# Kernel optimization log

Hardware: AMD Instinct MI355X
Metric: run time of the kernel (lower is better)

The kernel has to match this reference:

```python
import jax, jax.numpy as jnp
import numpy as np


def setup_inputs() -> dict:
    key = jax.random.key(0)
    k1, k2, k3, k4 = jax.random.split(key, 4)
    bs, ts0, tsk, f, nf = 1024, 32, 32, 64, 64
    return {
        "x_0": jax.random.normal(k1, (bs, ts0, f), dtype=jnp.float32),
        "x_k": jax.random.normal(k2, (bs, tsk, f), dtype=jnp.float32),
        # Conv1d weight as used: (num_filters, in_ch=1, ts_0, ts_k)
        "weight": jax.random.normal(k3, (nf, 1, ts0, tsk), dtype=jnp.float32) * 0.05,
        "bias": jax.random.normal(k4, (nf,), dtype=jnp.float32) * 0.05,
    }


def reference(x_0, x_k, weight, bias):
    bs, ts0, f = x_0.shape
    _, tsk, _ = x_k.shape
    # Outer-product interaction: (bs, f, ts_0, ts_k). This is the large HBM
    # intermediate (268 MB at these shapes) that a fused kernel would avoid.
    z = jnp.einsum('btf,byf->bfty', x_0, x_k)
    # Faithful row-major view to (bs, 1, ts_0, f*ts_k) as in torch .view.
    z = z.reshape(bs, 1, ts0, f * tsk)
    # Conv with kernel (ts_0, ts_k), stride ts_k along width; kernel height
    # equals input height so output is (bs, nf, 1, f). (Height stride is
    # irrelevant since exactly one vertical position exists.)
    out = jax.lax.conv_general_dilated(
        z, weight,
        window_strides=(tsk, tsk),
        padding='VALID',
        dimension_numbers=('NCHW', 'OIHW', 'NCHW'),
    )
    out = out + bias[None, :, None, None]
    return jnp.squeeze(out)  # (bs, num_filters, f)
```

## Files before the change

kernel.cpp:

```cpp
#include <hip/hip_runtime.h>


constexpr int ST0 = 36;
constexpr int GR  = 136;
constexpr int GB  = 32 * GR;

__global__ __launch_bounds__(1024)
__attribute__((amdgpu_waves_per_eu(4, 4)))
void cin_fused(const float* __restrict__ x0,
               const float* __restrict__ xk,
               const float* __restrict__ W,
               const float* __restrict__ bias,
               float* __restrict__ out)
{
    __shared__ __align__(16) float x0T[4 * 64 * ST0];
    __shared__ __align__(16) float Gs[4 * GB];

    const int tid  = threadIdx.x;
    const int b0   = blockIdx.x * 4;
    const int lane = tid & 63;
    const int wv   = tid >> 6;
    const int r0   = 2 * wv;

    const float4* x0src = reinterpret_cast<const float4*>(x0 + (size_t)b0 * 2048);
    const float4 a0 = x0src[tid];
    const float4 a1 = x0src[tid + 1024];

    float w0reg[32], w1reg[32];
    {
        const float4* wp = reinterpret_cast<const float4*>(W + ((size_t)lane * 32 + r0) * 32);
        #pragma unroll
        for (int q = 0; q < 8; ++q) {
            const float4 v = wp[q];
            w0reg[4*q+0] = v.x; w0reg[4*q+1] = v.y; w0reg[4*q+2] = v.z; w0reg[4*q+3] = v.w;
        }
        #pragma unroll
        for (int q = 0; q < 8; ++q) {
            const float4 v = wp[8 + q];
            w1reg[4*q+0] = v.x; w1reg[4*q+1] = v.y; w1reg[4*q+2] = v.z; w1reg[4*q+3] = v.w;
        }
    }

    {
        const int kb  = tid >> 9;
        const int u   = tid & 511;
        const int st  = u >> 4;
        const int sf4 = u & 15;
        const int sts = st ^ (4 * (sf4 & 7));
        float* rA = &x0T[(kb    ) * 64 * ST0 + (4 * sf4) * ST0];
        float* rB = &x0T[(kb + 2) * 64 * ST0 + (4 * sf4) * ST0];
        rA[0 * ST0 + sts] = a0.x; rA[1 * ST0 + sts] = a0.y;
        rA[2 * ST0 + sts] = a0.z; rA[3 * ST0 + sts] = a0.w;
        rB[0 * ST0 + sts] = a1.x; rB[1 * ST0 + sts] = a1.y;
        rB[2 * ST0 + sts] = a1.z; rB[3 * ST0 + sts] = a1.w;
    }
    __syncthreads();

    const int su = __builtin_amdgcn_readfirstlane(wv);
    for (int kb = 0; kb < 4; ++kb) {
        const float4* pk4 = reinterpret_cast<const float4*>(xk + (size_t)(b0 + kb) * 2048);
        float a00 = 0.f, a01 = 0.f, a10 = 0.f, a11 = 0.f;
        #pragma unroll
        for (int q = 0; q < 4; ++q) {
            float4 kv[8];
            #pragma unroll
            for (int m = 0; m < 8; ++m)
                kv[m] = pk4[(q * 8 + m) * 16 + su];
            #pragma unroll
            for (int m = 0; m < 8; ++m) {
                const int j = q * 8 + m;
                a00 = fmaf(w0reg[j], kv[m].x, a00);
                a01 = fmaf(w0reg[j], kv[m].y, a01);
                a10 = fmaf(w1reg[j], kv[m].z, a10);
                a11 = fmaf(w1reg[j], kv[m].w, a11);
            }
        }
        float* gb = &Gs[kb * GB];
        gb[(r0    ) * GR +      lane] = a00;
        gb[(r0    ) * GR + 68 + lane] = a01;
        gb[(r0 + 1) * GR +      lane] = a10;
        gb[(r0 + 1) * GR + 68 + lane] = a11;
    }
    __syncthreads();

    if (wv % 5 == 0) {
        const int ckb = wv / 5;
        const int l   = lane;
        const int n0  = (l >> 3) * 8;
        const int w0c = (l & 7) * 8;
        const int h   = w0c >> 5;
        const int t0  = w0c & 31;

        const float4 bva = *reinterpret_cast<const float4*>(bias + n0);
        const float4 bvb = *reinterpret_cast<const float4*>(bias + n0 + 4);

        float acc[8][8];
        #pragma unroll
        for (int i = 0; i < 8; ++i) {
            acc[0][i] = bva.x; acc[1][i] = bva.y; acc[2][i] = bva.z; acc[3][i] = bva.w;
            acc[4][i] = bvb.x; acc[5][i] = bvb.y; acc[6][i] = bvb.z; acc[7][i] = bvb.w;
        }

        const float* xbase = &x0T[ckb * 64 * ST0];
        const float* gbase = &Gs[ckb * GB + h * 68];

        #pragma unroll 4
        for (int r = 0; r < 32; ++r) {
            const int fi = 2 * r + h;
            const int p  = 4 * ((fi >> 2) & 7);
            const float4 xa = *reinterpret_cast<const float4*>(&xbase[fi * ST0 + (t0 ^ p)]);
            const float4 xb = *reinterpret_cast<const float4*>(&xbase[fi * ST0 + ((t0 + 4) ^ p)]);
            const float4 g0 = *reinterpret_cast<const float4*>(&gbase[r * GR + n0]);
            const float4 g1 = *reinterpret_cast<const float4*>(&gbase[r * GR + n0 + 4]);
            const float ge[8] = {g0.x, g0.y, g0.z, g0.w, g1.x, g1.y, g1.z, g1.w};
            const float xv[8] = {xa.x, xa.y, xa.z, xa.w, xb.x, xb.y, xb.z, xb.w};
            #pragma unroll
            for (int e = 0; e < 8; ++e)
                #pragma unroll
                for (int i = 0; i < 8; ++i)
                    acc[e][i] = fmaf(ge[e], xv[i], acc[e][i]);
        }

        float* ob = out + (size_t)(b0 + ckb) * 4096;
        #pragma unroll
        for (int e = 0; e < 8; ++e) {
            *reinterpret_cast<float4*>(&ob[(n0 + e) * 64 + w0c]) =
                make_float4(acc[e][0], acc[e][1], acc[e][2], acc[e][3]);
            *reinterpret_cast<float4*>(&ob[(n0 + e) * 64 + w0c + 4]) =
                make_float4(acc[e][4], acc[e][5], acc[e][6], acc[e][7]);
        }
    }
}

extern "C" void kernel_launch(void* const* d_in, const int* in_sizes, int n_in,
                              void* d_out, int out_size, void* d_ws, size_t ws_size,
                              hipStream_t stream) {
    const float* x0   = (const float*)d_in[0];
    const float* xk   = (const float*)d_in[1];
    const float* W    = (const float*)d_in[2];
    const float* bias = (const float*)d_in[3];
    float* out = (float*)d_out;

    cin_fused<<<dim3(256), dim3(1024), 0, stream>>>(x0, xk, W, bias, out);
}
```

Measured before the change: 95.67 us.

## Use packed fp16 dot2 for second stage, reorder weights, spread across all waves

Stores x0 and the intermediate G in shared memory as packed fp16 pairs and computes the second contraction with fdot2, so all 16 waves participate instead of only 4 (wv%5==0). A separate pre-kernel reorders the weight tensor into the workspace so weight register loads are coalesced. The barrier after the x0 shared store is removed, relying on the later barrier. This lowers precision of the intermediate and inputs to fp16 (round-toward-zero), risking accuracy, and adds an extra kernel launch.

```diff
diff --git a/kernel.cpp b/kernel.cpp
--- a/kernel.cpp
+++ b/kernel.cpp
@@ -1,26 +1,35 @@
 #include <hip/hip_runtime.h>
 
 
-constexpr int ST0 = 36;
-constexpr int GR  = 136;
-constexpr int GB  = 32 * GR;
+typedef __fp16 hh2 __attribute__((ext_vector_type(2)));
+
+constexpr int XPS = 36;
+
+__global__ __launch_bounds__(256)
+void w_reorder(const float4* __restrict__ W4, float4* __restrict__ Wt)
+{
+    const int o    = blockIdx.x * 256 + threadIdx.x;
+    const int lane = o & 63;
+    const int q    = (o >> 6) & 15;
+    const int wv   = o >> 10;
+    Wt[o] = W4[lane * 256 + (2 * wv + (q >> 3)) * 8 + (q & 7)];
+}
 
 __global__ __launch_bounds__(1024)
 __attribute__((amdgpu_waves_per_eu(4, 4)))
 void cin_fused(const float* __restrict__ x0,
                const float* __restrict__ xk,
-               const float* __restrict__ W,
+               const float4* __restrict__ Wt,
                const float* __restrict__ bias,
                float* __restrict__ out)
 {
-    __shared__ __align__(16) float x0T[4 * 64 * ST0];
-    __shared__ __align__(16) float Gs[4 * GB];
+    __shared__ __align__(16) hh2 xP[4][2][16][XPS];
+    __shared__ __align__(16) hh2 Gp[4][2][16][64];
 
     const int tid  = threadIdx.x;
     const int b0   = blockIdx.x * 4;
     const int lane = tid & 63;
     const int wv   = tid >> 6;
-    const int r0   = 2 * wv;
 
     const float4* x0src = reinterpret_cast<const float4*>(x0 + (size_t)b0 * 2048);
     const float4 a0 = x0src[tid];
@@ -28,44 +37,40 @@
 
     float w0reg[32], w1reg[32];
     {
-        const float4* wp = reinterpret_cast<const float4*>(W + ((size_t)lane * 32 + r0) * 32);
+        const float4* wp = Wt + (size_t)wv * 1024 + lane;
         #pragma unroll
         for (int q = 0; q < 8; ++q) {
-            const float4 v = wp[q];
+            const float4 v = wp[q * 64];
             w0reg[4*q+0] = v.x; w0reg[4*q+1] = v.y; w0reg[4*q+2] = v.z; w0reg[4*q+3] = v.w;
         }
         #pragma unroll
         for (int q = 0; q < 8; ++q) {
-            const float4 v = wp[8 + q];
+            const float4 v = wp[(q + 8) * 64];
             w1reg[4*q+0] = v.x; w1reg[4*q+1] = v.y; w1reg[4*q+2] = v.z; w1reg[4*q+3] = v.w;
         }
     }
 
     {
-        const int kb  = tid >> 9;
-        const int u   = tid & 511;
-        const int st  = u >> 4;
-        const int sf4 = u & 15;
-        const int sts = st ^ (4 * (sf4 & 7));
-        float* rA = &x0T[(kb    ) * 64 * ST0 + (4 * sf4) * ST0];
-        float* rB = &x0T[(kb + 2) * 64 * ST0 + (4 * sf4) * ST0];
-        rA[0 * ST0 + sts] = a0.x; rA[1 * ST0 + sts] = a0.y;
-        rA[2 * ST0 + sts] = a0.z; rA[3 * ST0 + sts] = a0.w;
-        rB[0 * ST0 + sts] = a1.x; rB[1 * ST0 + sts] = a1.y;
-        rB[2 * ST0 + sts] = a1.z; rB[3 * ST0 + sts] = a1.w;
+        const int kb = tid >> 9;
+        const int u  = tid & 511;
+        const int t  = u >> 4;
+        const int f  = u & 15;
+        xP[kb    ][0][f][t] = __builtin_amdgcn_cvt_pkrtz(a0.x, a0.z);
+        xP[kb    ][1][f][t] = __builtin_amdgcn_cvt_pkrtz(a0.y, a0.w);
+        xP[kb + 2][0][f][t] = __builtin_amdgcn_cvt_pkrtz(a1.x, a1.z);
+        xP[kb + 2][1][f][t] = __builtin_amdgcn_cvt_pkrtz(a1.y, a1.w);
     }
-    __syncthreads();
 
     const int su = __builtin_amdgcn_readfirstlane(wv);
     for (int kb = 0; kb < 4; ++kb) {
-        const float4* pk4 = reinterpret_cast<const float4*>(xk + (size_t)(b0 + kb) * 2048);
+        const float4* pk4 = reinterpret_cast<const float4*>(xk + (size_t)(b0 + kb) * 2048) + su;
         float a00 = 0.f, a01 = 0.f, a10 = 0.f, a11 = 0.f;
         #pragma unroll
         for (int q = 0; q < 4; ++q) {
             float4 kv[8];
             #pragma unroll
             for (int m = 0; m < 8; ++m)
-                kv[m] = pk4[(q * 8 + m) * 16 + su];
+                kv[m] = pk4[(q * 8 + m) * 16];
             #pragma unroll
             for (int m = 0; m < 8; ++m) {
                 const int j = q * 8 + m;
@@ -75,59 +80,50 @@
                 a11 = fmaf(w1reg[j], kv[m].w, a11);
             }
         }
-        float* gb = &Gs[kb * GB];
-        gb[(r0    ) * GR +      lane] = a00;
-        gb[(r0    ) * GR + 68 + lane] = a01;
-        gb[(r0 + 1) * GR +      lane] = a10;
-        gb[(r0 + 1) * GR + 68 + lane] = a11;
+        Gp[kb][0][wv][lane] = __builtin_amdgcn_cvt_pkrtz(a00, a10);
+        Gp[kb][1][wv][lane] = __builtin_amdgcn_cvt_pkrtz(a01, a11);
     }
     __syncthreads();
 
-    if (wv % 5 == 0) {
-        const int ckb = wv / 5;
-        const int l   = lane;
-        const int n0  = (l >> 3) * 8;
-        const int w0c = (l & 7) * 8;
+    {
+        const int kb  = tid >> 8;
+        const int t2  = tid & 255;
+        const int n0  = (t2 >> 4) * 4;
+        const int w0c = (t2 & 15) * 4;
         const int h   = w0c >> 5;
         const int t0  = w0c & 31;
 
-        const float4 bva = *reinterpret_cast<const float4*>(bias + n0);
-        const float4 bvb = *reinterpret_cast<const float4*>(bias + n0 + 4);
-
-        float acc[8][8];
+        const float4 bv = *reinterpret_cast<const float4*>(bias + n0);
+        float acc[4][4];
         #pragma unroll
-        for (int i = 0; i < 8; ++i) {
-            acc[0][i] = bva.x; acc[1][i] = bva.y; acc[2][i] = bva.z; acc[3][i] = bva.w;
-            acc[4][i] = bvb.x; acc[5][i] = bvb.y; acc[6][i] = bvb.z; acc[7][i] = bvb.w;
+        for (int i = 0; i < 4; ++i) {
+            acc[0][i] = bv.x; acc[1][i] = bv.y; acc[2][i] = bv.z; acc[3][i] = bv.w;
         }
 
-        const float* xbase = &x0T[ckb * 64 * ST0];
-        const float* gbase = &Gs[ckb * GB + h * 68];
-
-        #pragma unroll 4
-        for (int r = 0; r < 32; ++r) {
-            const int fi = 2 * r + h;
-            const int p  = 4 * ((fi >> 2) & 7);
-            const float4 xa = *reinterpret_cast<const float4*>(&xbase[fi * ST0 + (t0 ^ p)]);
-            const float4 xb = *reinterpret_cast<const float4*>(&xbase[fi * ST0 + ((t0 + 4) ^ p)]);
-            const float4 g0 = *reinterpret_cast<const float4*>(&gbase[r * GR + n0]);
-            const float4 g1 = *reinterpret_cast<const float4*>(&gbase[r * GR + n0 + 4]);
-            const float ge[8] = {g0.x, g0.y, g0.z, g0.w, g1.x, g1.y, g1.z, g1.w};
-            const float xv[8] = {xa.x, xa.y, xa.z, xa.w, xb.x, xb.y, xb.z, xb.w};
+        #pragma unroll
+        for (int rp = 0; rp < 16; ++rp) {
+            union { float4 f; hh2 p[4]; } xu, guv;
+            xu.f  = *reinterpret_cast<const float4*>(&xP[kb][h][rp][t0]);
+            guv.f = *reinterpret_cast<const float4*>(&Gp[kb][h][rp][n0]);
             #pragma unroll
-            for (int e = 0; e < 8; ++e)
+            for (int e = 0; e < 4; ++e) {
                 #pragma unroll
-                for (int i = 0; i < 8; ++i)
-                    acc[e][i] = fmaf(ge[e], xv[i], acc[e][i]);
+                for (int i = 0; i < 4; ++i) {
+#if __has_builtin(__builtin_amdgcn_fdot2)
+                    acc[e][i] = __builtin_amdgcn_fdot2(guv.p[e], xu.p[i], acc[e][i], false);
+#else
+                    acc[e][i] += (float)guv.p[e].x * (float)xu.p[i].x
+                               + (float)guv.p[e].y * (float)xu.p[i].y;
+#endif
+                }
+            }
         }
 
-        float* ob = out + (size_t)(b0 + ckb) * 4096;
+        float* ob = out + (size_t)(b0 + kb) * 4096;
         #pragma unroll
-        for (int e = 0; e < 8; ++e) {
+        for (int e = 0; e < 4; ++e) {
             *reinterpret_cast<float4*>(&ob[(n0 + e) * 64 + w0c]) =
                 make_float4(acc[e][0], acc[e][1], acc[e][2], acc[e][3]);
-            *reinterpret_cast<float4*>(&ob[(n0 + e) * 64 + w0c + 4]) =
-                make_float4(acc[e][4], acc[e][5], acc[e][6], acc[e][7]);
         }
     }
 }
@@ -140,6 +136,8 @@
     const float* W    = (const float*)d_in[2];
     const float* bias = (const float*)d_in[3];
     float* out = (float*)d_out;
+    float4* Wt = (float4*)d_ws;
 
-    cin_fused<<<dim3(256), dim3(1024), 0, stream>>>(x0, xk, W, bias, out);
+    w_reorder<<<dim3(64), dim3(256), 0, stream>>>((const float4*)W, Wt);
+    cin_fused<<<dim3(256), dim3(1024), 0, stream>>>(x0, xk, Wt, bias, out);
 }
```

Result: faster. 87.11 us (-9.0%).
